# Kernel optimization log

Measured on AMD Instinct MI355X. Metric: run time of the kernel, lower is better.

The kernel has to match this reference:

```python
import jax, jax.numpy as jnp
import numpy as np

T, B, NIN, N, A = 100, 32, 512, 2048, 2
DT = 1e-3
THR = 1.0
ALPHA = float(np.exp(-DT / 0.01))


def setup_inputs() -> dict:
    key = jax.random.key(0)
    k1, k2, k3, k4 = jax.random.split(key, 4)
    rates = jax.random.uniform(k1, (T, B, NIN), dtype=jnp.float32) * 100.0  # Hz
    noise = jax.random.uniform(k2, (T, B, NIN), dtype=jnp.float32)  # Poisson thresholds
    Win = jax.random.normal(k3, (A, NIN, N), dtype=jnp.float32) * (1.5 / np.sqrt(NIN))
    Wrec = jax.random.normal(k4, (A, A, N, N), dtype=jnp.float32) * (1.0 / np.sqrt(N))
    return {"rates": rates, "noise": noise, "Win": Win, "Wrec": Wrec}


def reference(rates, noise, Win, Wrec):
    dtype = rates.dtype
    V0 = jnp.zeros((A, B, N), dtype)   # membrane potentials, all areas
    Xd0 = jnp.zeros((A, B, N), dtype)  # delayed cross-area spikes (reset())

    def step(carry, inp):
        V, Xd = carry
        rate_t, noise_t = inp
        # PoissonInput: Bernoulli spikes with prob rate*dt
        Xi = (noise_t < rate_t * DT).astype(dtype)  # [B, NIN]
        # per-area input current: feedforward + all-to-all cross-area recurrent
        I = jnp.einsum('bi,ain->abn', Xi, Win) + jnp.einsum('sbn,sanm->abm', Xd, Wrec)
        # LIF: leak, reset on previous spike, integrate
        V_new = ALPHA * V * (1.0 - Xd) + I
        S = (V_new >= THR).astype(dtype)  # [A, B, N]
        return (V_new, S), (Xi, S)

    (_, _), (Xis, Ss) = jax.lax.scan(step, (V0, Xd0), (rates, noise))
    # Xis: [T, B, NIN]; Ss: [T, A, B, N] -> per-area stacked outputs
    return (Xis, Ss[:, 0], Ss[:, 1])
```

## Files before the change

kernel.cpp:

```cpp
#include <hip/hip_runtime.h>

#define T_STEPS 100
#define BATCH   32
#define NIN     512
#define NN      2048
#define AREAS   2

#define ALPHA_D 0.9048374180359595

__global__ __launch_bounds__(256)
void k0_xi(const float* __restrict__ rates, const float* __restrict__ noise,
           float* __restrict__ outXi, unsigned* __restrict__ xi_mask)
{
    int el = blockIdx.x * 256 + threadIdx.x;
    float r = rates[el], nz = noise[el];
    float p = __fmul_rn(r, 0.001f);
    int spike = (nz < p) ? 1 : 0;
    outXi[el] = (float)spike;
    if (spike) {
        int t = el >> 14;
        int b = (el >> 9) & 31;
        int i = el & (NIN - 1);
        atomicOr(&xi_mask[(t * 32 + b) * 16 + (i >> 5)], 1u << (i & 31));
    }
}

__global__ __launch_bounds__(256)
void k_ff(const float* __restrict__ Win, const unsigned* __restrict__ xi_mask,
          float* __restrict__ Iff)
{
    const int tb  = blockIdx.x;
    const int a   = blockIdx.y;
    const int tid = threadIdx.x;

    __shared__ unsigned mws[16];
    if (tid < 16) mws[tid] = xi_mask[tb * 16 + tid];
    __syncthreads();

    const float* Wa = Win + ((size_t)a << 20) + (tid << 3);
    float4 A0 = {0,0,0,0}, A1 = {0,0,0,0};
    for (int w = 0; w < 16; ++w) {
        unsigned mw = mws[w];
        int base_i = w << 5;
        while (mw) {
            int i = base_i + (__ffs(mw) - 1);
            mw &= mw - 1;
            const float* rp = Wa + ((size_t)i << 11);
            float4 w0 = ((const float4*)rp)[0];
            float4 w1 = ((const float4*)rp)[1];
            A0.x += w0.x; A0.y += w0.y; A0.z += w0.z; A0.w += w0.w;
            A1.x += w1.x; A1.y += w1.y; A1.z += w1.z; A1.w += w1.w;
        }
    }
    float* op = Iff + (((size_t)tb * 2 + a) << 11) + (tid << 3);
    ((float4*)op)[0] = A0;
    ((float4*)op)[1] = A1;
}

#define OFF_OF(rr) ((((rr) >> 11) << 23) + (((rr) & 2047) << 11))

__device__ __forceinline__ void issue8v(const float* __restrict__ Wa,
                                        const unsigned short* lp, float4* p)
{
    uint4 u = *(const uint4*)lp;
    p[0] = *(const float4*)(Wa + OFF_OF((int)(u.x & 0xffff)));
    p[1] = *(const float4*)(Wa + OFF_OF((int)(u.x >> 16)));
    p[2] = *(const float4*)(Wa + OFF_OF((int)(u.y & 0xffff)));
    p[3] = *(const float4*)(Wa + OFF_OF((int)(u.y >> 16)));
    p[4] = *(const float4*)(Wa + OFF_OF((int)(u.z & 0xffff)));
    p[5] = *(const float4*)(Wa + OFF_OF((int)(u.z >> 16)));
    p[6] = *(const float4*)(Wa + OFF_OF((int)(u.w & 0xffff)));
    p[7] = *(const float4*)(Wa + OFF_OF((int)(u.w >> 16)));
}

#define ACC4(P)  { acc.x = __fadd_rn(acc.x, (P).x); acc.y = __fadd_rn(acc.y, (P).y); \
                   acc.z = __fadd_rn(acc.z, (P).z); acc.w = __fadd_rn(acc.w, (P).w); }

__global__ __launch_bounds__(64, 1)
void k_steps(const float* __restrict__ Wrec,
             unsigned long long* __restrict__ smask,
             const float* __restrict__ Iff,
             float* __restrict__ outS)
{
    const int lane = threadIdx.x;
    const int bx   = blockIdx.x;
    const int s    = bx & 15;
    const int b    = bx >> 4;
    const int a    = s >> 3;
    const int m0   = (s & 7) << 8;
    const int c    = m0 + (lane << 2);

    __shared__ unsigned mws[128];
    __shared__ __align__(16) unsigned short lrec[AREAS * NN];
    __shared__ int base[128];
    __shared__ int cnt_rec;
    __shared__ unsigned nsp[8];

    const float* __restrict__ Wa = Wrec + ((size_t)a << 22) + c;
    const int rr_self = (a << 11) | c;
    const int wsel = rr_self >> 5;
    const int bsh  = rr_self & 31;
    const int w0   = s << 3;

    float4 vst = {0.f, 0.f, 0.f, 0.f};

    for (int t = 0; t < T_STEPS; ++t) {
        unsigned long long* cur = smask + (size_t)(t & 1) * (BATCH * 128) + (b << 7);
        unsigned long long* nxt = smask + (size_t)((t + 1) & 1) * (BATCH * 128) + (b << 7);

        {
            unsigned long long v0 = __hip_atomic_load(&cur[lane], __ATOMIC_RELAXED,
                                                      __HIP_MEMORY_SCOPE_AGENT);
            while ((unsigned)(v0 >> 32) != (unsigned)t) {
                __builtin_amdgcn_s_sleep(2);
                v0 = __hip_atomic_load(&cur[lane], __ATOMIC_RELAXED,
                                       __HIP_MEMORY_SCOPE_AGENT);
            }
            unsigned long long v1 = __hip_atomic_load(&cur[lane + 64], __ATOMIC_RELAXED,
                                                      __HIP_MEMORY_SCOPE_AGENT);
            while ((unsigned)(v1 >> 32) != (unsigned)t) {
                __builtin_amdgcn_s_sleep(2);
                v1 = __hip_atomic_load(&cur[lane + 64], __ATOMIC_RELAXED,
                                       __HIP_MEMORY_SCOPE_AGENT);
            }
            mws[lane]      = (unsigned)v0;
            mws[lane + 64] = (unsigned)v1;
        }
        if (lane < 8) nsp[lane] = 0u;
        float4 accf = *(const float4*)
            &Iff[((((size_t)t * BATCH + b) * 2 + a) << 11) + c];
        __syncthreads();

        {
            int c0 = __popc(mws[2 * lane]), c1 = __popc(mws[2 * lane + 1]);
            int cc = c0 + c1, incl = cc;
            #pragma unroll
            for (int d = 1; d < 64; d <<= 1) {
                int v = __shfl_up(incl, d, 64);
                if (lane >= d) incl += v;
            }
            base[2 * lane]     = incl - cc;
            base[2 * lane + 1] = incl - c1;
            if (lane == 63) cnt_rec = incl;
        }
        __syncthreads();

        {
            unsigned w = mws[2 * lane];
            int off = base[2 * lane];
            int bb = (2 * lane) << 5;
            while (w) { int p = __ffs(w) - 1; lrec[off++] = (unsigned short)(bb + p); w &= w - 1; }
            w = mws[2 * lane + 1];
            off = base[2 * lane + 1];
            bb = (2 * lane + 1) << 5;
            while (w) { int p = __ffs(w) - 1; lrec[off++] = (unsigned short)(bb + p); w &= w - 1; }
        }
        __syncthreads();

        const int nrec = cnt_rec;
        unsigned xw = (mws[wsel] >> bsh) & 0xFu;

        float4 acc = {0.f, 0.f, 0.f, 0.f};
        int j = 0;
        if (nrec >= 16) {
            float4 p[16], q[16];
            issue8v(Wa, &lrec[0], p); issue8v(Wa, &lrec[8], p + 8);
            j = 16;
            while (j + 32 <= nrec) {
                issue8v(Wa, &lrec[j], q); issue8v(Wa, &lrec[j + 8], q + 8);
                __builtin_amdgcn_sched_barrier(0);
                #pragma unroll
                for (int k = 0; k < 16; ++k) ACC4(p[k]);
                issue8v(Wa, &lrec[j + 16], p); issue8v(Wa, &lrec[j + 24], p + 8);
                __builtin_amdgcn_sched_barrier(0);
                #pragma unroll
                for (int k = 0; k < 16; ++k) ACC4(q[k]);
                j += 32;
            }
            if (j + 16 <= nrec) {
                issue8v(Wa, &lrec[j], q); issue8v(Wa, &lrec[j + 8], q + 8);
                __builtin_amdgcn_sched_barrier(0);
                #pragma unroll
                for (int k = 0; k < 16; ++k) ACC4(p[k]);
                #pragma unroll
                for (int k = 0; k < 16; ++k) p[k] = q[k];
                j += 16;
            }
            #pragma unroll
            for (int k = 0; k < 16; ++k) ACC4(p[k]);
        }
        if (nrec - j >= 8) {
            float4 p8[8];
            issue8v(Wa, &lrec[j], p8);
            #pragma unroll
            for (int k = 0; k < 8; ++k) ACC4(p8[k]);
            j += 8;
        }
        for (; j < nrec; ++j) {
            float4 pr = *(const float4*)(Wa + OFF_OF((int)lrec[j]));
            ACC4(pr);
        }

        float4 sv;
        unsigned nib = 0u;
#define LIF(K, BIT) { \
            float v  = __fmul_rn((float)ALPHA_D, vst.K); \
            if (xw & BIT) v = 0.0f; \
            float I  = __fadd_rn(accf.K, acc.K); \
            float vn = __fadd_rn(v, I); \
            vst.K = vn; \
            if (vn >= 1.0f) { sv.K = 1.0f; nib |= BIT; } else sv.K = 0.0f; \
        }
        LIF(x, 1u) LIF(y, 2u) LIF(z, 4u) LIF(w, 8u)
#undef LIF
        if (nib) atomicOr(&nsp[lane >> 3], nib << ((lane & 7) << 2));
        __syncthreads();

        if (t < T_STEPS - 1 && lane < 8) {
            unsigned long long pv =
                ((unsigned long long)(unsigned)(t + 1) << 32) | nsp[lane];
            atomicExch(&nxt[w0 + lane], pv);
        }
        *(float4*)&outS[(size_t)a * (T_STEPS * BATCH * NN)
                        + (((size_t)t * BATCH + b) << 11) + c] = sv;
    }
}
#undef OFF_OF
#undef ACC4

extern "C" void kernel_launch(void* const* d_in, const int* in_sizes, int n_in,
                              void* d_out, int out_size, void* d_ws, size_t ws_size,
                              hipStream_t stream)
{
    const float* rates = (const float*)d_in[0];
    const float* noise = (const float*)d_in[1];
    const float* Win   = (const float*)d_in[2];
    const float* Wrec  = (const float*)d_in[3];
    float* out = (float*)d_out;

    char* ws = (char*)d_ws;
    unsigned* xi_mask = (unsigned*)ws;
    unsigned long long* smask = (unsigned long long*)(ws + 204800);
    float* Iff = (float*)(ws + 270336);

    hipMemsetAsync(d_ws, 0, 270336, stream);

    k0_xi<<<6400, 256, 0, stream>>>(rates, noise, out, xi_mask);
    k_ff<<<dim3(3200, 2), 256, 0, stream>>>(Win, xi_mask, Iff);

    float* outS = out + (size_t)T_STEPS * BATCH * NIN;
    void* args[] = { (void*)&Wrec, (void*)&smask, (void*)&Iff, (void*)&outS };
    hipLaunchCooperativeKernel((const void*)k_steps, dim3(512), dim3(64),
                               args, 0, stream);
}
```

Measured before the change: 1.236 ms.

## Gather recurrent weight rows via global_load_lds staging instead of register prefetch

Replaces the register-double-buffered float4 gather of spiking Wrec rows with direct global-to-LDS loads (global_load_lds, 16 bytes per lane) into a 64-row shared staging buffer. After a vmcnt(0) wait, the rows are read back from LDS and accumulated. The aim is more loads in flight without the register pressure of the p/q arrays. In exchange it adds 64 KB of LDS, a full drain per 64-row chunk with no overlap between chunks, and an extra LDS read pass. The LDS destination addressing assumes per-lane 16-byte placement semantics, and accumulation order is unchanged.

```diff
diff --git a/kernel.cpp b/kernel.cpp
--- a/kernel.cpp
+++ b/kernel.cpp
@@ -59,19 +59,9 @@
 
 #define OFF_OF(rr) ((((rr) >> 11) << 23) + (((rr) & 2047) << 11))
 
-__device__ __forceinline__ void issue8v(const float* __restrict__ Wa,
-                                        const unsigned short* lp, float4* p)
-{
-    uint4 u = *(const uint4*)lp;
-    p[0] = *(const float4*)(Wa + OFF_OF((int)(u.x & 0xffff)));
-    p[1] = *(const float4*)(Wa + OFF_OF((int)(u.x >> 16)));
-    p[2] = *(const float4*)(Wa + OFF_OF((int)(u.y & 0xffff)));
-    p[3] = *(const float4*)(Wa + OFF_OF((int)(u.y >> 16)));
-    p[4] = *(const float4*)(Wa + OFF_OF((int)(u.z & 0xffff)));
-    p[5] = *(const float4*)(Wa + OFF_OF((int)(u.z >> 16)));
-    p[6] = *(const float4*)(Wa + OFF_OF((int)(u.w & 0xffff)));
-    p[7] = *(const float4*)(Wa + OFF_OF((int)(u.w >> 16)));
-}
+#define GLDS(src, dst) __builtin_amdgcn_global_load_lds(                      \
+    (const __attribute__((address_space(1))) void*)(src),                     \
+    (__attribute__((address_space(3))) void*)(dst), 16, 0, 0)
 
 #define ACC4(P)  { acc.x = __fadd_rn(acc.x, (P).x); acc.y = __fadd_rn(acc.y, (P).y); \
                    acc.z = __fadd_rn(acc.z, (P).z); acc.w = __fadd_rn(acc.w, (P).w); }
@@ -90,13 +80,14 @@
     const int m0   = (s & 7) << 8;
     const int c    = m0 + (lane << 2);
 
+    __shared__ __align__(16) float stage[64 * 256];
     __shared__ unsigned mws[128];
     __shared__ __align__(16) unsigned short lrec[AREAS * NN];
     __shared__ int base[128];
     __shared__ int cnt_rec;
     __shared__ unsigned nsp[8];
 
-    const float* __restrict__ Wa = Wrec + ((size_t)a << 22) + c;
+    const float* __restrict__ Wb = Wrec + ((size_t)a << 22) + m0 + (lane << 2);
     const int rr_self = (a << 11) | c;
     const int wsel = rr_self >> 5;
     const int bsh  = rr_self & 31;
@@ -161,44 +152,37 @@
         unsigned xw = (mws[wsel] >> bsh) & 0xFu;
 
         float4 acc = {0.f, 0.f, 0.f, 0.f};
-        int j = 0;
-        if (nrec >= 16) {
-            float4 p[16], q[16];
-            issue8v(Wa, &lrec[0], p); issue8v(Wa, &lrec[8], p + 8);
-            j = 16;
-            while (j + 32 <= nrec) {
-                issue8v(Wa, &lrec[j], q); issue8v(Wa, &lrec[j + 8], q + 8);
-                __builtin_amdgcn_sched_barrier(0);
-                #pragma unroll
-                for (int k = 0; k < 16; ++k) ACC4(p[k]);
-                issue8v(Wa, &lrec[j + 16], p); issue8v(Wa, &lrec[j + 24], p + 8);
-                __builtin_amdgcn_sched_barrier(0);
-                #pragma unroll
-                for (int k = 0; k < 16; ++k) ACC4(q[k]);
-                j += 32;
-            }
-            if (j + 16 <= nrec) {
-                issue8v(Wa, &lrec[j], q); issue8v(Wa, &lrec[j + 8], q + 8);
-                __builtin_amdgcn_sched_barrier(0);
-                #pragma unroll
-                for (int k = 0; k < 16; ++k) ACC4(p[k]);
-                #pragma unroll
-                for (int k = 0; k < 16; ++k) p[k] = q[k];
-                j += 16;
-            }
-            #pragma unroll
-            for (int k = 0; k < 16; ++k) ACC4(p[k]);
-        }
-        if (nrec - j >= 8) {
-            float4 p8[8];
-            issue8v(Wa, &lrec[j], p8);
-            #pragma unroll
-            for (int k = 0; k < 8; ++k) ACC4(p8[k]);
-            j += 8;
-        }
-        for (; j < nrec; ++j) {
-            float4 pr = *(const float4*)(Wa + OFF_OF((int)lrec[j]));
-            ACC4(pr);
+        for (int j = 0; j < nrec; j += 64) {
+            const int cnt = min(64, nrec - j);
+            int k = 0;
+            for (; k + 8 <= cnt; k += 8) {
+                uint4 u0 = *(const uint4*)&lrec[j + k];
+                GLDS(Wb + OFF_OF((int)(u0.x & 0xffff)), &stage[(k + 0) << 8]);
+                GLDS(Wb + OFF_OF((int)(u0.x >> 16)),    &stage[(k + 1) << 8]);
+                GLDS(Wb + OFF_OF((int)(u0.y & 0xffff)), &stage[(k + 2) << 8]);
+                GLDS(Wb + OFF_OF((int)(u0.y >> 16)),    &stage[(k + 3) << 8]);
+                GLDS(Wb + OFF_OF((int)(u0.z & 0xffff)), &stage[(k + 4) << 8]);
+                GLDS(Wb + OFF_OF((int)(u0.z >> 16)),    &stage[(k + 5) << 8]);
+                GLDS(Wb + OFF_OF((int)(u0.w & 0xffff)), &stage[(k + 6) << 8]);
+                GLDS(Wb + OFF_OF((int)(u0.w >> 16)),    &stage[(k + 7) << 8]);
+            }
+            for (; k < cnt; ++k) {
+                int row = lrec[j + k];
+                GLDS(Wb + OFF_OF(row), &stage[k << 8]);
+            }
+            asm volatile("s_waitcnt vmcnt(0)" ::: "memory");
+            __builtin_amdgcn_sched_barrier(0);
+            for (k = 0; k + 4 <= cnt; k += 4) {
+                float4 w0 = *(const float4*)&stage[((k + 0) << 8) + (lane << 2)];
+                float4 w1 = *(const float4*)&stage[((k + 1) << 8) + (lane << 2)];
+                float4 w2 = *(const float4*)&stage[((k + 2) << 8) + (lane << 2)];
+                float4 w3 = *(const float4*)&stage[((k + 3) << 8) + (lane << 2)];
+                ACC4(w0); ACC4(w1); ACC4(w2); ACC4(w3);
+            }
+            for (; k < cnt; ++k) {
+                float4 w = *(const float4*)&stage[(k << 8) + (lane << 2)];
+                ACC4(w);
+            }
         }
 
         float4 sv;
@@ -227,6 +211,7 @@
 }
 #undef OFF_OF
 #undef ACC4
+#undef GLDS
 
 extern "C" void kernel_launch(void* const* d_in, const int* in_sizes, int n_in,
                               void* d_out, int out_size, void* d_ws, size_t ws_size,
```

New measurement: 1.389 ms. 12.4% more time.
